# Performance work log

Measured on AMD Instinct MI355X. Metric: run time of the kernel, lower is better.

Reference implementation:

```python
import jax, jax.numpy as jnp
import numpy as np

DIM = 512
NUM_HEADS = 8
HEAD_DIM = DIM // NUM_HEADS
SCALE = HEAD_DIM ** -0.5


def setup_inputs() -> dict:
    key = jax.random.key(0)
    k_x, k_qkv, k_o, k_ob = jax.random.split(key, 4)
    b, c, h, w = 2, DIM, 64, 64
    x = jax.random.normal(k_x, (b, c, h, w), dtype=jnp.float32)
    # torch nn.Linear weight layout: [out_features, in_features]
    w_qkv = jax.random.normal(k_qkv, (3 * DIM, DIM), dtype=jnp.float32) * (DIM ** -0.5)
    w_out = jax.random.normal(k_o, (DIM, DIM), dtype=jnp.float32) * (DIM ** -0.5)
    b_out = jax.random.normal(k_ob, (DIM,), dtype=jnp.float32) * 0.01
    return {"x": x, "w_qkv": w_qkv, "w_out": w_out, "b_out": b_out}


def reference(x, w_qkv, w_out, b_out):
    b, c, h, w = x.shape
    s = h * w
    # [b, c, h, w] -> [b, s, c]
    xs = x.reshape(b, c, s).transpose(0, 2, 1)
    qkv = xs @ w_qkv.T                      # [b, s, 3c]
    q, k, v = jnp.split(qkv, 3, axis=-1)    # each [b, s, c]

    def to_heads(t):
        return t.reshape(b, s, NUM_HEADS, HEAD_DIM).transpose(0, 2, 1, 3)  # [b, H, s, d]

    q, k, v = map(to_heads, (q, k, v))
    dots = jnp.einsum('bhqd,bhkd->bhqk', q, k) * SCALE   # [b, H, s, s]
    attn = jax.nn.softmax(dots, axis=-1)
    out = jnp.einsum('bhqk,bhkd->bhqd', attn, v)          # [b, H, s, d]
    out = out.transpose(0, 2, 1, 3).reshape(b, s, c)      # [b, s, c]
    out = out @ w_out.T + b_out                            # output projection
    return out.transpose(0, 2, 1).reshape(b, c, h, w)
```

## Files before the change

### kernel.cpp

```cpp
#include <hip/hip_runtime.h>
#include <hip/hip_bf16.h>

#define B 2
#define C 512
#define H 8
#define D 64
#define S 4096
#define O3 1536
#define E2 0.18033688011112042f
#define THR_RAW 64.0f

#define XT_OFF 0ull
#define WQ_OFF 4194304ull
#define WO_OFF 4980736ull
#define Q_OFF  5242880ull
#define K_OFF  9437184ull
#define V_OFF  13631488ull
#define AO_OFF 17825792ull

typedef __attribute__((ext_vector_type(8))) short bf16x8;
typedef __attribute__((ext_vector_type(4))) float f32x4;

__device__ __forceinline__ ushort f2bf(float f) {
    __hip_bfloat16 h = __float2bfloat16(f);
    return *reinterpret_cast<ushort*>(&h);
}

__global__ __launch_bounds__(256) void transpose_x(const float* __restrict__ x,
                                                   ushort* __restrict__ xT) {
    const int s0 = blockIdx.x * 64, c0 = blockIdx.y * 64, b = blockIdx.z;
    const int tid = threadIdx.x;
    __shared__ float T[64][68];

    const float* xb = x + (size_t)b * C * S;
    #pragma unroll
    for (int i = 0; i < 4; ++i) {
        int idx = tid + i * 256;
        int row = idx >> 4, sv = idx & 15;
        *(float4*)&T[row][sv * 4] =
            *(const float4*)&xb[(size_t)(c0 + row) * S + s0 + sv * 4];
    }
    __syncthreads();
    #pragma unroll
    for (int i = 0; i < 2; ++i) {
        int idx = tid + i * 256;
        int orow = idx >> 3, och = idx & 7;
        ushort tmp[8];
        #pragma unroll
        for (int j = 0; j < 8; ++j) tmp[j] = f2bf(T[och * 8 + j][orow]);
        ushort* dst = &xT[((size_t)b * S + s0 + orow) * C + c0 + och * 8];
        *(ushort4*)&dst[0] = *(ushort4*)&tmp[0];
        *(ushort4*)&dst[4] = *(ushort4*)&tmp[4];
    }
}

__global__ __launch_bounds__(256) void conv_bf16(const float* __restrict__ src,
                                                 ushort* __restrict__ dst, int n4) {
    int idx = blockIdx.x * 256 + threadIdx.x;
    if (idx < n4) {
        float4 v = *(const float4*)&src[(size_t)idx * 4];
        ushort4 o = {f2bf(v.x), f2bf(v.y), f2bf(v.z), f2bf(v.w)};
        *(ushort4*)&dst[(size_t)idx * 4] = o;
    }
}

__global__ __launch_bounds__(256) void qkv_mfma(const ushort* __restrict__ xT,
                                                const ushort* __restrict__ wq,
                                                ushort* __restrict__ ws) {
    const int m0 = blockIdx.x * 128;
    const int o0 = blockIdx.y * 128;
    const int b  = blockIdx.z;
    const int tid = threadIdx.x;
    const int w = tid >> 6, l = tid & 63;
    const int l15 = l & 15, l4 = l >> 4;
    const int wr = w >> 1, wc = w & 1;

    __shared__ __align__(16) ushort At[128][72];
    __shared__ __align__(16) ushort Bt[128][72];

    const ushort* Ag = xT + ((size_t)b * S + m0) * C;
    const ushort* Bg = wq + (size_t)o0 * C;

    f32x4 acc[4][4];
    #pragma unroll
    for (int i = 0; i < 4; ++i)
        #pragma unroll
        for (int j = 0; j < 4; ++j) acc[i][j] = (f32x4){0.f, 0.f, 0.f, 0.f};

    for (int k0 = 0; k0 < C; k0 += 64) {
        if (k0) __syncthreads();
        #pragma unroll
        for (int i = 0; i < 4; ++i) {
            int idx = tid + i * 256;
            int row = idx >> 3, ch = idx & 7;
            *(bf16x8*)&At[row][ch * 8] =
                *(const bf16x8*)&Ag[(size_t)row * C + k0 + ch * 8];
            *(bf16x8*)&Bt[row][ch * 8] =
                *(const bf16x8*)&Bg[(size_t)row * C + k0 + ch * 8];
        }
        __syncthreads();
        #pragma unroll
        for (int c = 0; c < 2; ++c) {
            bf16x8 af[4], bfr[4];
            #pragma unroll
            for (int i = 0; i < 4; ++i) {
                af[i]  = *(const bf16x8*)&At[wr * 64 + i * 16 + l15][c * 32 + l4 * 8];
                bfr[i] = *(const bf16x8*)&Bt[wc * 64 + i * 16 + l15][c * 32 + l4 * 8];
            }
            #pragma unroll
            for (int i = 0; i < 4; ++i)
                #pragma unroll
                for (int j = 0; j < 4; ++j)
                    acc[i][j] = __builtin_amdgcn_mfma_f32_16x16x32_bf16(
                        af[i], bfr[j], acc[i][j], 0, 0, 0);
        }
    }

    const int t = o0 >> 9;
    #pragma unroll
    for (int j = 0; j < 4; ++j) {
        const int ob = o0 + wc * 64 + j * 16;
        const int h  = (ob & 511) >> 6;
        const int d0 = (ob & 63) + l15;
        if (t < 2) {
            ushort* dst = ws + (t == 0 ? Q_OFF : K_OFF) + (size_t)(b * H + h) * S * D;
            #pragma unroll
            for (int i = 0; i < 4; ++i) {
                #pragma unroll
                for (int r = 0; r < 4; ++r) {
                    int m = m0 + wr * 64 + i * 16 + l4 * 4 + r;
                    dst[(size_t)m * D + d0] = f2bf(acc[i][j][r]);
                }
            }
        } else {
            ushort* dst = ws + V_OFF + (size_t)(b * H + h) * D * S + (size_t)d0 * S;
            #pragma unroll
            for (int i = 0; i < 4; ++i) {
                int m = m0 + wr * 64 + i * 16 + l4 * 4;
                ushort4 pk = {f2bf(acc[i][j][0]), f2bf(acc[i][j][1]),
                              f2bf(acc[i][j][2]), f2bf(acc[i][j][3])};
                *(ushort4*)&dst[m] = pk;
            }
        }
    }
}

__global__ __launch_bounds__(256) void attn_kernel(const ushort* __restrict__ wsb,
                                                   ushort* __restrict__ aob) {
    const int q0 = blockIdx.x * 64;
    const int h  = blockIdx.y;
    const int b  = blockIdx.z;
    const int tid = threadIdx.x;
    const int w   = tid >> 6;
    const int l   = tid & 63;
    const int l15 = l & 15, l4 = l >> 4;

    const size_t bh = (size_t)(b * H + h);
    const ushort* qg = wsb + Q_OFF + bh * S * D;
    const ushort* kg = wsb + K_OFF + bh * S * D;
    const ushort* vg = wsb + V_OFF + bh * D * S;

    __shared__ __align__(16) ushort Kt[128][72];
    __shared__ __align__(16) ushort Vt[64][136];

    bf16x8 b_q[2];
    {
        int row = q0 + w * 16 + l15;
        b_q[0] = *(const bf16x8*)&qg[(size_t)row * D + l4 * 8];
        b_q[1] = *(const bf16x8*)&qg[(size_t)row * D + 32 + l4 * 8];
    }

    f32x4 o_acc[4];
    #pragma unroll
    for (int dt = 0; dt < 4; ++dt) o_acc[dt] = (f32x4){0.f, 0.f, 0.f, 0.f};
    float m_run = -1e30f, l_run = 0.f;

    const f32x4 zero4 = (f32x4){0.f, 0.f, 0.f, 0.f};

    const int krow = tid >> 3, kch = tid & 7;
    const int vrow = tid >> 4, vtch = tid & 15;
    const int vc = vtch >> 2, vl4 = vtch & 3;

    bf16x8 kst[4];
    ushort4 vst[4][2];

    #pragma unroll
    for (int p = 0; p < 4; ++p) {
        kst[p] = *(const bf16x8*)&kg[(size_t)(krow + p * 32) * D + kch * 8];
        #pragma unroll
        for (int jj = 0; jj < 2; ++jj)
            vst[p][jj] = *(const ushort4*)&vg[(size_t)(vrow + p * 16) * S +
                                              (2 * vc + jj) * 16 + vl4 * 4];
    }

    const int NT = S / 128;
    for (int kt = 0; kt < NT; ++kt) {
        #pragma unroll
        for (int p = 0; p < 4; ++p) {
            *(bf16x8*)&Kt[krow + p * 32][kch * 8] = kst[p];
            #pragma unroll
            for (int jj = 0; jj < 2; ++jj)
                *(ushort4*)&Vt[vrow + p * 16][vtch * 8 + jj * 4] = vst[p][jj];
        }
        __syncthreads();

        if (kt + 1 < NT) {
            #pragma unroll
            for (int p = 0; p < 4; ++p) {
                kst[p] = *(const bf16x8*)&kg[(size_t)((kt + 1) * 128 + krow + p * 32) * D + kch * 8];
                #pragma unroll
                for (int jj = 0; jj < 2; ++jj)
                    vst[p][jj] = *(const ushort4*)&vg[(size_t)(vrow + p * 16) * S +
                                                      (kt + 1) * 128 + (2 * vc + jj) * 16 + vl4 * 4];
            }
        }

        f32x4 s[8];
        __builtin_amdgcn_s_setprio(1);
        #pragma unroll
        for (int nt = 0; nt < 8; ++nt) {
            bf16x8 ak0 = *(const bf16x8*)&Kt[nt * 16 + l15][l4 * 8];
            bf16x8 ak1 = *(const bf16x8*)&Kt[nt * 16 + l15][32 + l4 * 8];
            f32x4 t = __builtin_amdgcn_mfma_f32_16x16x32_bf16(ak0, b_q[0], zero4, 0, 0, 0);
            s[nt] = __builtin_amdgcn_mfma_f32_16x16x32_bf16(ak1, b_q[1], t, 0, 0, 0);
        }
        __builtin_amdgcn_s_setprio(0);

        float mt = s[0][0];
        #pragma unroll
        for (int nt = 0; nt < 8; ++nt)
            #pragma unroll
            for (int reg = 0; reg < 4; ++reg) mt = fmaxf(mt, s[nt][reg]);
        mt = fmaxf(mt, __shfl_xor(mt, 16, 64));
        mt = fmaxf(mt, __shfl_xor(mt, 32, 64));

        bool ok = (mt <= m_run + THR_RAW);
        if (!__all(ok)) {
            float mn = fmaxf(m_run, mt);
            float alpha = __builtin_amdgcn_exp2f((m_run - mn) * E2);
            m_run = mn;
            l_run *= alpha;
            #pragma unroll
            for (int dt = 0; dt < 4; ++dt)
                #pragma unroll
                for (int reg = 0; reg < 4; ++reg) o_acc[dt][reg] *= alpha;
        }

        float msc = m_run * E2;
        float lt = 0.f;
        #pragma unroll
        for (int nt = 0; nt < 8; ++nt)
            #pragma unroll
            for (int reg = 0; reg < 4; ++reg) {
                float p = __builtin_amdgcn_exp2f(fmaf(s[nt][reg], E2, -msc));
                s[nt][reg] = p;
                lt += p;
            }
        lt += __shfl_xor(lt, 16, 64);
        lt += __shfl_xor(lt, 32, 64);
        l_run += lt;

        unsigned int pw[8][2];
        #pragma unroll
        for (int nt = 0; nt < 8; ++nt)
            #pragma unroll
            for (int rp = 0; rp < 2; ++rp)
                pw[nt][rp] = (unsigned int)f2bf(s[nt][2 * rp]) |
                             ((unsigned int)f2bf(s[nt][2 * rp + 1]) << 16);

        __builtin_amdgcn_s_setprio(1);
        #pragma unroll
        for (int c = 0; c < 4; ++c) {
            union { unsigned int u[4]; bf16x8 v; } pbu;
            pbu.u[0] = pw[2 * c][0];
            pbu.u[1] = pw[2 * c][1];
            pbu.u[2] = pw[2 * c + 1][0];
            pbu.u[3] = pw[2 * c + 1][1];
            #pragma unroll
            for (int dt = 0; dt < 4; ++dt) {
                bf16x8 av = *(const bf16x8*)&Vt[dt * 16 + l15][c * 32 + l4 * 8];
                o_acc[dt] = __builtin_amdgcn_mfma_f32_16x16x32_bf16(
                    av, pbu.v, o_acc[dt], 0, 0, 0);
            }
        }
        __builtin_amdgcn_s_setprio(0);
        __syncthreads();
    }

    float inv = 1.0f / l_run;
    int row = q0 + w * 16 + l15;
    #pragma unroll
    for (int dt = 0; dt < 4; ++dt) {
        ushort4 pk = {f2bf(o_acc[dt][0] * inv), f2bf(o_acc[dt][1] * inv),
                      f2bf(o_acc[dt][2] * inv), f2bf(o_acc[dt][3] * inv)};
        *(ushort4*)&aob[((size_t)b * S + row) * C + h * 64 + dt * 16 + l4 * 4] = pk;
    }
}

__global__ __launch_bounds__(256) void oproj_mfma(const ushort* __restrict__ wo,
                                                  const ushort* __restrict__ aob,
                                                  const float* __restrict__ b_out,
                                                  float* __restrict__ out) {
    const int cc0 = blockIdx.x * 128;
    const int n0  = blockIdx.y * 128;
    const int b   = blockIdx.z;
    const int tid = threadIdx.x;
    const int w = tid >> 6, l = tid & 63;
    const int l15 = l & 15, l4 = l >> 4;
    const int wr = w >> 1, wc = w & 1;

    __shared__ __align__(16) ushort At[128][72];
    __shared__ __align__(16) ushort Bt[128][72];

    const ushort* Ag = wo + (size_t)cc0 * C;
    const ushort* Bg = aob + ((size_t)b * S + n0) * C;

    f32x4 acc[4][4];
    #pragma unroll
    for (int i = 0; i < 4; ++i)
        #pragma unroll
        for (int j = 0; j < 4; ++j) acc[i][j] = (f32x4){0.f, 0.f, 0.f, 0.f};

    for (int k0 = 0; k0 < C; k0 += 64) {
        if (k0) __syncthreads();
        #pragma unroll
        for (int i = 0; i < 4; ++i) {
            int idx = tid + i * 256;
            int row = idx >> 3, ch = idx & 7;
            *(bf16x8*)&At[row][ch * 8] =
                *(const bf16x8*)&Ag[(size_t)row * C + k0 + ch * 8];
            *(bf16x8*)&Bt[row][ch * 8] =
                *(const bf16x8*)&Bg[(size_t)row * C + k0 + ch * 8];
        }
        __syncthreads();
        #pragma unroll
        for (int c = 0; c < 2; ++c) {
            bf16x8 af[4], bfr[4];
            #pragma unroll
            for (int i = 0; i < 4; ++i) {
                af[i]  = *(const bf16x8*)&At[wr * 64 + i * 16 + l15][c * 32 + l4 * 8];
                bfr[i] = *(const bf16x8*)&Bt[wc * 64 + i * 16 + l15][c * 32 + l4 * 8];
            }
            #pragma unroll
            for (int i = 0; i < 4; ++i)
                #pragma unroll
                for (int j = 0; j < 4; ++j)
                    acc[i][j] = __builtin_amdgcn_mfma_f32_16x16x32_bf16(
                        af[i], bfr[j], acc[i][j], 0, 0, 0);
        }
    }

    #pragma unroll
    for (int i = 0; i < 4; ++i) {
        #pragma unroll
        for (int r = 0; r < 4; ++r) {
            int cc = cc0 + wr * 64 + i * 16 + l4 * 4 + r;
            float bias = b_out[cc];
            #pragma unroll
            for (int j = 0; j < 4; ++j) {
                int mm = n0 + wc * 64 + j * 16 + l15;
                out[((size_t)b * C + cc) * S + mm] = acc[i][j][r] + bias;
            }
        }
    }
}

extern "C" void kernel_launch(void* const* d_in, const int* in_sizes, int n_in,
                              void* d_out, int out_size, void* d_ws, size_t ws_size,
                              hipStream_t stream) {
    (void)in_sizes; (void)n_in; (void)out_size; (void)ws_size;
    const float* x     = (const float*)d_in[0];
    const float* w_qkv = (const float*)d_in[1];
    const float* w_out = (const float*)d_in[2];
    const float* b_out = (const float*)d_in[3];
    float* out = (float*)d_out;
    ushort* wsb = (ushort*)d_ws;

    transpose_x<<<dim3(S / 64, C / 64, B), 256, 0, stream>>>(x, wsb + XT_OFF);
    conv_bf16<<<dim3((O3 * C / 4 + 255) / 256), 256, 0, stream>>>(w_qkv, wsb + WQ_OFF, O3 * C / 4);
    conv_bf16<<<dim3((C * C / 4 + 255) / 256), 256, 0, stream>>>(w_out, wsb + WO_OFF, C * C / 4);
    qkv_mfma<<<dim3(S / 128, O3 / 128, B), 256, 0, stream>>>(wsb + XT_OFF, wsb + WQ_OFF, wsb);
    attn_kernel<<<dim3(S / 64, H, B), 256, 0, stream>>>(wsb, wsb + AO_OFF);
    oproj_mfma<<<dim3(C / 128, S / 128, B), 256, 0, stream>>>(wsb + WO_OFF, wsb + AO_OFF, b_out, out);
}
```

Baseline: 195.2 us.

## Process two query sub-tiles per wave in attention and compute row sums via MFMA

Each attention block now handles 128 queries instead of 64, with each wave owning two 16-row query sub-tiles that share every K and V tile load from shared memory. This halves the number of blocks and the global and LDS K/V traffic per query. The softmax row sum is now accumulated with an extra MFMA against a vector of bf16 ones instead of scalar adds and shuffles, and probabilities are packed with a paired bf16 conversion. The cost is higher register pressure from doubled accumulators, which may reduce occupancy, and only 512 blocks are launched.

```diff
diff --git a/kernel.cpp b/kernel.cpp
--- a/kernel.cpp
+++ b/kernel.cpp
@@ -24,6 +24,11 @@
 __device__ __forceinline__ ushort f2bf(float f) {
     __hip_bfloat16 h = __float2bfloat16(f);
     return *reinterpret_cast<ushort*>(&h);
+}
+
+__device__ __forceinline__ unsigned pack2bf(float lo, float hi) {
+    __hip_bfloat162 h = __float22bfloat162_rn(float2{lo, hi});
+    return *reinterpret_cast<unsigned*>(&h);
 }
 
 __global__ __launch_bounds__(256) void transpose_x(const float* __restrict__ x,
@@ -147,7 +152,7 @@
 
 __global__ __launch_bounds__(256) void attn_kernel(const ushort* __restrict__ wsb,
                                                    ushort* __restrict__ aob) {
-    const int q0 = blockIdx.x * 64;
+    const int q0 = blockIdx.x * 128;
     const int h  = blockIdx.y;
     const int b  = blockIdx.z;
     const int tid = threadIdx.x;
@@ -163,19 +168,28 @@
     __shared__ __align__(16) ushort Kt[128][72];
     __shared__ __align__(16) ushort Vt[64][136];
 
-    bf16x8 b_q[2];
-    {
-        int row = q0 + w * 16 + l15;
-        b_q[0] = *(const bf16x8*)&qg[(size_t)row * D + l4 * 8];
-        b_q[1] = *(const bf16x8*)&qg[(size_t)row * D + 32 + l4 * 8];
-    }
-
-    f32x4 o_acc[4];
-    #pragma unroll
-    for (int dt = 0; dt < 4; ++dt) o_acc[dt] = (f32x4){0.f, 0.f, 0.f, 0.f};
-    float m_run = -1e30f, l_run = 0.f;
+    bf16x8 b_q[2][2];
+    #pragma unroll
+    for (int sub = 0; sub < 2; ++sub) {
+        int row = q0 + w * 32 + sub * 16 + l15;
+        b_q[sub][0] = *(const bf16x8*)&qg[(size_t)row * D + l4 * 8];
+        b_q[sub][1] = *(const bf16x8*)&qg[(size_t)row * D + 32 + l4 * 8];
+    }
+
+    f32x4 o_acc[2][4], o_sum[2];
+    float m_run[2];
+    #pragma unroll
+    for (int sub = 0; sub < 2; ++sub) {
+        #pragma unroll
+        for (int dt = 0; dt < 4; ++dt) o_acc[sub][dt] = (f32x4){0.f, 0.f, 0.f, 0.f};
+        o_sum[sub] = (f32x4){0.f, 0.f, 0.f, 0.f};
+        m_run[sub] = -1e30f;
+    }
 
     const f32x4 zero4 = (f32x4){0.f, 0.f, 0.f, 0.f};
+    const short one_bf = (short)0x3F80;
+    const bf16x8 ones8 = {one_bf, one_bf, one_bf, one_bf,
+                          one_bf, one_bf, one_bf, one_bf};
 
     const int krow = tid >> 3, kch = tid & 7;
     const int vrow = tid >> 4, vtch = tid & 15;
@@ -215,85 +229,104 @@
             }
         }
 
-        f32x4 s[8];
+        f32x4 s[2][8];
         __builtin_amdgcn_s_setprio(1);
         #pragma unroll
         for (int nt = 0; nt < 8; ++nt) {
             bf16x8 ak0 = *(const bf16x8*)&Kt[nt * 16 + l15][l4 * 8];
             bf16x8 ak1 = *(const bf16x8*)&Kt[nt * 16 + l15][32 + l4 * 8];
-            f32x4 t = __builtin_amdgcn_mfma_f32_16x16x32_bf16(ak0, b_q[0], zero4, 0, 0, 0);
-            s[nt] = __builtin_amdgcn_mfma_f32_16x16x32_bf16(ak1, b_q[1], t, 0, 0, 0);
+            #pragma unroll
+            for (int sub = 0; sub < 2; ++sub) {
+                f32x4 t = __builtin_amdgcn_mfma_f32_16x16x32_bf16(ak0, b_q[sub][0], zero4, 0, 0, 0);
+                s[sub][nt] = __builtin_amdgcn_mfma_f32_16x16x32_bf16(ak1, b_q[sub][1], t, 0, 0, 0);
+            }
         }
         __builtin_amdgcn_s_setprio(0);
 
-        float mt = s[0][0];
-        #pragma unroll
-        for (int nt = 0; nt < 8; ++nt)
-            #pragma unroll
-            for (int reg = 0; reg < 4; ++reg) mt = fmaxf(mt, s[nt][reg]);
-        mt = fmaxf(mt, __shfl_xor(mt, 16, 64));
-        mt = fmaxf(mt, __shfl_xor(mt, 32, 64));
-
-        bool ok = (mt <= m_run + THR_RAW);
+        float mt[2];
+        #pragma unroll
+        for (int sub = 0; sub < 2; ++sub) {
+            float m4[8];
+            #pragma unroll
+            for (int nt = 0; nt < 8; ++nt)
+                m4[nt] = fmaxf(fmaxf(s[sub][nt][0], s[sub][nt][1]),
+                               fmaxf(s[sub][nt][2], s[sub][nt][3]));
+            float a = fmaxf(fmaxf(m4[0], m4[1]), fmaxf(m4[2], m4[3]));
+            float c = fmaxf(fmaxf(m4[4], m4[5]), fmaxf(m4[6], m4[7]));
+            float m0 = fmaxf(a, c);
+            m0 = fmaxf(m0, __shfl_xor(m0, 16, 64));
+            m0 = fmaxf(m0, __shfl_xor(m0, 32, 64));
+            mt[sub] = m0;
+        }
+
+        bool ok = (mt[0] <= m_run[0] + THR_RAW) && (mt[1] <= m_run[1] + THR_RAW);
         if (!__all(ok)) {
-            float mn = fmaxf(m_run, mt);
-            float alpha = __builtin_amdgcn_exp2f((m_run - mn) * E2);
-            m_run = mn;
-            l_run *= alpha;
-            #pragma unroll
-            for (int dt = 0; dt < 4; ++dt)
-                #pragma unroll
-                for (int reg = 0; reg < 4; ++reg) o_acc[dt][reg] *= alpha;
-        }
-
-        float msc = m_run * E2;
-        float lt = 0.f;
-        #pragma unroll
-        for (int nt = 0; nt < 8; ++nt)
-            #pragma unroll
-            for (int reg = 0; reg < 4; ++reg) {
-                float p = __builtin_amdgcn_exp2f(fmaf(s[nt][reg], E2, -msc));
-                s[nt][reg] = p;
-                lt += p;
-            }
-        lt += __shfl_xor(lt, 16, 64);
-        lt += __shfl_xor(lt, 32, 64);
-        l_run += lt;
-
-        unsigned int pw[8][2];
-        #pragma unroll
-        for (int nt = 0; nt < 8; ++nt)
-            #pragma unroll
-            for (int rp = 0; rp < 2; ++rp)
-                pw[nt][rp] = (unsigned int)f2bf(s[nt][2 * rp]) |
-                             ((unsigned int)f2bf(s[nt][2 * rp + 1]) << 16);
+            #pragma unroll
+            for (int sub = 0; sub < 2; ++sub) {
+                float mn = fmaxf(m_run[sub], mt[sub]);
+                float alpha = __builtin_amdgcn_exp2f((m_run[sub] - mn) * E2);
+                m_run[sub] = mn;
+                o_sum[sub] *= alpha;
+                #pragma unroll
+                for (int dt = 0; dt < 4; ++dt) o_acc[sub][dt] *= alpha;
+            }
+        }
+
+        unsigned pw[2][8][2];
+        #pragma unroll
+        for (int sub = 0; sub < 2; ++sub) {
+            float msc = m_run[sub] * E2;
+            #pragma unroll
+            for (int nt = 0; nt < 8; ++nt) {
+                float p0 = __builtin_amdgcn_exp2f(fmaf(s[sub][nt][0], E2, -msc));
+                float p1 = __builtin_amdgcn_exp2f(fmaf(s[sub][nt][1], E2, -msc));
+                float p2 = __builtin_amdgcn_exp2f(fmaf(s[sub][nt][2], E2, -msc));
+                float p3 = __builtin_amdgcn_exp2f(fmaf(s[sub][nt][3], E2, -msc));
+                pw[sub][nt][0] = pack2bf(p0, p1);
+                pw[sub][nt][1] = pack2bf(p2, p3);
+            }
+        }
 
         __builtin_amdgcn_s_setprio(1);
         #pragma unroll
         for (int c = 0; c < 4; ++c) {
-            union { unsigned int u[4]; bf16x8 v; } pbu;
-            pbu.u[0] = pw[2 * c][0];
-            pbu.u[1] = pw[2 * c][1];
-            pbu.u[2] = pw[2 * c + 1][0];
-            pbu.u[3] = pw[2 * c + 1][1];
+            bf16x8 pb[2];
+            #pragma unroll
+            for (int sub = 0; sub < 2; ++sub) {
+                union { unsigned u[4]; bf16x8 v; } pbu;
+                pbu.u[0] = pw[sub][2 * c][0];
+                pbu.u[1] = pw[sub][2 * c][1];
+                pbu.u[2] = pw[sub][2 * c + 1][0];
+                pbu.u[3] = pw[sub][2 * c + 1][1];
+                pb[sub] = pbu.v;
+            }
             #pragma unroll
             for (int dt = 0; dt < 4; ++dt) {
                 bf16x8 av = *(const bf16x8*)&Vt[dt * 16 + l15][c * 32 + l4 * 8];
-                o_acc[dt] = __builtin_amdgcn_mfma_f32_16x16x32_bf16(
-                    av, pbu.v, o_acc[dt], 0, 0, 0);
-            }
+                #pragma unroll
+                for (int sub = 0; sub < 2; ++sub)
+                    o_acc[sub][dt] = __builtin_amdgcn_mfma_f32_16x16x32_bf16(
+                        av, pb[sub], o_acc[sub][dt], 0, 0, 0);
+            }
+            #pragma unroll
+            for (int sub = 0; sub < 2; ++sub)
+                o_sum[sub] = __builtin_amdgcn_mfma_f32_16x16x32_bf16(
+                    ones8, pb[sub], o_sum[sub], 0, 0, 0);
         }
         __builtin_amdgcn_s_setprio(0);
         __syncthreads();
     }
 
-    float inv = 1.0f / l_run;
-    int row = q0 + w * 16 + l15;
-    #pragma unroll
-    for (int dt = 0; dt < 4; ++dt) {
-        ushort4 pk = {f2bf(o_acc[dt][0] * inv), f2bf(o_acc[dt][1] * inv),
-                      f2bf(o_acc[dt][2] * inv), f2bf(o_acc[dt][3] * inv)};
-        *(ushort4*)&aob[((size_t)b * S + row) * C + h * 64 + dt * 16 + l4 * 4] = pk;
+    #pragma unroll
+    for (int sub = 0; sub < 2; ++sub) {
+        float inv = 1.0f / o_sum[sub][0];
+        int row = q0 + w * 32 + sub * 16 + l15;
+        #pragma unroll
+        for (int dt = 0; dt < 4; ++dt) {
+            ushort4 pk = {f2bf(o_acc[sub][dt][0] * inv), f2bf(o_acc[sub][dt][1] * inv),
+                          f2bf(o_acc[sub][dt][2] * inv), f2bf(o_acc[sub][dt][3] * inv)};
+            *(ushort4*)&aob[((size_t)b * S + row) * C + h * 64 + dt * 16 + l4 * 4] = pk;
+        }
     }
 }
 
@@ -380,6 +413,6 @@
     conv_bf16<<<dim3((O3 * C / 4 + 255) / 256), 256, 0, stream>>>(w_qkv, wsb + WQ_OFF, O3 * C / 4);
     conv_bf16<<<dim3((C * C / 4 + 255) / 256), 256, 0, stream>>>(w_out, wsb + WO_OFF, C * C / 4);
     qkv_mfma<<<dim3(S / 128, O3 / 128, B), 256, 0, stream>>>(wsb + XT_OFF, wsb + WQ_OFF, wsb);
-    attn_kernel<<<dim3(S / 64, H, B), 256, 0, stream>>>(wsb, wsb + AO_OFF);
+    attn_kernel<<<dim3(S / 128, H, B), 256, 0, stream>>>(wsb, wsb + AO_OFF);
     oproj_mfma<<<dim3(C / 128, S / 128, B), 256, 0, stream>>>(wsb + WO_OFF, wsb + AO_OFF, b_out, out);
 }
```

New measurement: 205.3 us. 1.05x slower.
